# Kernel optimization log

Measured on AMD Instinct MI355X. Metric: run time of the kernel, lower is better.

The kernel has to match this reference:

```python
import jax, jax.numpy as jnp
import numpy as np

DN = ('NCHW', 'OIHW', 'NCHW')
EPS = 1e-5

def _conv(x, w, stride, padding):
    return jax.lax.conv_general_dilated(x, w, stride, padding, dimension_numbers=DN)

def _bn(x, g, b, m, v):
    # inference-mode BatchNorm2d
    s = g * jax.lax.rsqrt(v + EPS)
    return x * s[None, :, None, None] + (b - m * s)[None, :, None, None]

def _gn(x, g, b, groups):
    B, C, H, W = x.shape
    xr = x.reshape(B, groups, -1)
    mu = xr.mean(axis=2, keepdims=True)
    var = xr.var(axis=2, keepdims=True)
    xn = ((xr - mu) * jax.lax.rsqrt(var + EPS)).reshape(B, C, H, W)
    return xn * g[None, :, None, None] + b[None, :, None, None]

def _dsconv(f, ow, ob, og, obb, om, ov, w, wb, gg, gb, morph, k=3, extend_scope=1.0):
    B, C, H, W = f.shape
    S = H  # source DSC coordinate map only type-checks for square inputs
    off = jnp.tanh(_bn(_conv(f, ow, (1, 1), [(1, 1), (1, 1)]) + ob[None, :, None, None], og, obb, om, ov))
    # source passes y_offset for morph 0, x_offset for morph 1; both are added to y_new
    sel = off[:, :k] if morph == 0 else off[:, k:]
    center = k // 2
    # _apply_offset: detached clone, center zeroed; cumulative loop is empty for k=3
    off_cum = jax.lax.stop_gradient(sel).at[:, center].set(0.0) * extend_scope
    vals = jnp.linspace(float((-k) // 2), float(k // 2), k, dtype=f.dtype)  # [-2,-0.5,1] for k=3 (source quirk)
    rowc = jnp.arange(S, dtype=f.dtype)[:, None]  # both y_center and x_center equal the row index
    yg = jnp.zeros((k,), f.dtype) if morph == 0 else vals
    xg = vals if morph == 0 else jnp.zeros((k,), f.dtype)
    y = rowc[None, None] + yg[None, :, None, None] + off_cum                       # (B,k,S,S)
    x = jnp.broadcast_to(rowc[None, None] + xg[None, :, None, None], (B, k, S, S))
    rs = lambda t: t.transpose(0, 2, 1, 3).reshape(B, k * S, S)  # b p w h -> b (w p) h
    y, x = rs(y), rs(x)
    y0 = jnp.clip(jnp.floor(y), 0, S - 1); y1 = jnp.clip(jnp.floor(y) + 1.0, 0, S - 1)
    x0 = jnp.clip(jnp.floor(x), 0, S - 1); x1 = jnp.clip(jnp.floor(x) + 1.0, 0, S - 1)
    # source: index_a0 = base_y0 - base + x0  (batch offset cancels -> all batches gather from batch 0)
    flat0 = f[0].transpose(1, 2, 0).reshape(S * S, C)
    gat = lambda yy, xx: flat0[(yy * S + xx).astype(jnp.int32)]  # (B,kS,S,C)
    out = (gat(y0, x0) * ((y1 - y) * (x1 - x))[..., None]
         + gat(y0, x1) * ((y1 - y) * (x - x0))[..., None]
         + gat(y1, x0) * ((y - y0) * (x1 - x))[..., None]
         + gat(y1, x1) * ((y - y0) * (x - x0))[..., None])
    if morph == 0:
        df = out.transpose(0, 3, 1, 2)                    # (B,C,k*S,S)
        z = _conv(df, w, (k, 1), 'VALID')
    else:
        df = out.reshape(B, S, k * S, C).transpose(0, 3, 1, 2)  # (B,C,S,k*S)
        z = _conv(df, w, (1, k), 'VALID')
    z = z + wb[None, :, None, None]
    return jax.nn.silu(_gn(z, gg, gb, w.shape[0] // 4))

def _forward(x, w0, g0, b0, m0, v0,
             owx, obx, ogx, obbx, omx, ovx, wx, bwx, ggx, gbx,
             owy, oby, ogy, obby, omy, ovy, wy, bwy, ggy, gby):
    out0 = jax.nn.silu(_bn(_conv(x, w0, (1, 1), [(1, 1), (1, 1)]), g0, b0, m0, v0))
    outx = _dsconv(x, owx, obx, ogx, obbx, omx, ovx, wx, bwx, ggx, gbx, morph=0)
    outy = _dsconv(x, owy, oby, ogy, obby, omy, ovy, wy, bwy, ggy, gby, morph=1)
    return jnp.concatenate([out0, outx, outy], axis=1)

def setup_inputs() -> dict:
    B, C, O, S, K = 4, 64, 64, 256, 3
    key = jax.random.key(0)
    ks = jax.random.split(key, 32)
    rn = lambda i, sh, sc=1.0: jax.random.normal(ks[i], sh, dtype=jnp.float32) * sc
    ru = lambda i, sh: jax.random.uniform(ks[i], sh, dtype=jnp.float32) + 0.5
    return {
        'x': rn(0, (B, C, S, S)),
        'w0': rn(1, (O, C, 3, 3), 0.05), 'g0': ru(2, (O,)), 'b0': rn(3, (O,), 0.1),
        'm0': rn(4, (O,), 0.1), 'v0': ru(5, (O,)),
        'owx': rn(6, (2 * K, C, 3, 3), 0.05), 'obx': rn(7, (2 * K,), 0.1),
        'ogx': ru(8, (2 * K,)), 'obbx': rn(9, (2 * K,), 0.1), 'omx': rn(10, (2 * K,), 0.1), 'ovx': ru(11, (2 * K,)),
        'wx': rn(12, (O, C, K, 1), 0.05), 'bwx': rn(13, (O,), 0.1), 'ggx': ru(14, (O,)), 'gbx': rn(15, (O,), 0.1),
        'owy': rn(16, (2 * K, C, 3, 3), 0.05), 'oby': rn(17, (2 * K,), 0.1),
        'ogy': ru(18, (2 * K,)), 'obby': rn(19, (2 * K,), 0.1), 'omy': rn(20, (2 * K,), 0.1), 'ovy': ru(21, (2 * K,)),
        'wy': rn(22, (O, C, 1, K), 0.05), 'bwy': rn(23, (O,), 0.1), 'ggy': ru(24, (O,)), 'gby': rn(25, (O,), 0.1),
    }

def reference(x, w0, g0, b0, m0, v0,
              owx, obx, ogx, obbx, omx, ovx, wx, bwx, ggx, gbx,
              owy, oby, ogy, obby, omy, ovy, wy, bwy, ggy, gby):
    return _forward(x, w0, g0, b0, m0, v0,
                    owx, obx, ogx, obbx, omx, ovx, wx, bwx, ggx, gbx,
                    owy, oby, ogy, obby, omy, ovy, wy, bwy, ggy, gby)
```

## Files before the change

kernel.cpp:

```cpp
#include <hip/hip_runtime.h>
#include <hip/hip_bf16.h>
#include <math.h>

#define TS 256
#define HW 65536
#define CIN 64
#define EPSV 1e-5f
#define XPITCH 258

typedef __attribute__((ext_vector_type(8))) short bf16x8;
typedef __attribute__((ext_vector_type(4))) float f32x4;
typedef __attribute__((ext_vector_type(4))) unsigned short u16x4;
typedef unsigned short ushort_t;

__device__ __forceinline__ float silu_f(float v){ return v / (1.0f + expf(-v)); }
__device__ __forceinline__ ushort_t f2bf(float f){
    __hip_bfloat16 h = __float2bfloat16(f);
    return *reinterpret_cast<ushort_t*>(&h);
}
__device__ __forceinline__ float bf2f(ushort_t u){
    unsigned int t = ((unsigned int)u) << 16;
    return __uint_as_float(t);
}

__global__ __launch_bounds__(256) void k_xbf(const float* __restrict__ x, ushort_t* __restrict__ xbf){
    __shared__ float tile[64][65];
    int blk = blockIdx.x;
    int b = blk >> 10;
    int chunk = blk & 1023;
    int p0 = chunk * 64;
    int i = p0 >> 8, jb = p0 & 255;
    int tid = threadIdx.x;
    int lane = tid & 63, grp = tid >> 6;
    #pragma unroll
    for (int k = 0; k < 16; ++k){
        int c = k*4 + grp;
        tile[lane][c] = x[((size_t)(b*CIN + c))*HW + p0 + lane];
    }
    __syncthreads();
    #pragma unroll
    for (int k = 0; k < 16; ++k){
        int pp = k*4 + grp;
        xbf[(((size_t)b*258 + (i+1))*XPITCH + 1 + jb + pp)*64 + lane] = f2bf(tile[pp][lane]);
    }
}

__global__ void k_halo(ushort_t* __restrict__ xbf){
    int r = blockIdx.x;
    int b = blockIdx.y;
    int t = threadIdx.x;
    size_t rowbase = ((size_t)b*258 + r)*XPITCH*64;
    if (r == 0 || r == 257){
        for (int idx = t; idx < XPITCH*64; idx += 256) xbf[rowbase + idx] = 0;
    } else {
        if (t < 64) xbf[rowbase + t] = 0;
        else if (t < 128) xbf[rowbase + (size_t)257*64 + (t-64)] = 0;
    }
}

__global__ __launch_bounds__(256) void k_wrepack(const float* __restrict__ w0, ushort_t* __restrict__ w0bf){
    int idx = blockIdx.x*256 + threadIdx.x;
    int r = idx >> 12;
    int rem = idx & 4095;
    int o = rem >> 6, c = rem & 63;
    w0bf[idx] = f2bf(w0[(o*64 + c)*9 + r]);
}

__global__ __launch_bounds__(256) void k_wdsc(const float* __restrict__ wx, const float* __restrict__ wy,
        ushort_t* __restrict__ wbfx, ushort_t* __restrict__ wbfy){
    int idx = blockIdx.x*256 + threadIdx.x;
    int set = idx / 12288;
    int rem = idx - set*12288;
    int o = rem / 192;
    int k = rem - o*192;
    int t = k >> 6, c = k & 63;
    const float* w = set ? wy : wx;
    ushort_t* dst = set ? wbfy : wbfx;
    dst[rem] = f2bf(w[(o*64 + c)*3 + t]);
}

__global__ __launch_bounds__(256) void k_offp(const float* __restrict__ x,
        const float* __restrict__ owx, const float* __restrict__ owy,
        float* __restrict__ poff){
    __shared__ float xs[8][4][258];
    __shared__ float wsm[4][8][9];
    int by = blockIdx.y;
    int b = by >> 3, chunk = by & 7;
    int i0 = blockIdx.x * 2;
    int tid = threadIdx.x;
    for (int idx = tid; idx < 4*8*9; idx += 256){
        int o = idx / 72;
        int rem = idx - o*72;
        int c = rem / 9, tap = rem - c*9;
        int morph = o >> 1;
        int ch = (o==0)?0:(o==1)?2:(o==2)?3:5;
        const float* w = morph ? owy : owx;
        wsm[o][c][tap] = w[(ch*64 + chunk*8 + c)*9 + tap];
    }
    for (int idx = tid; idx < 8*4*258; idx += 256){
        int c = idx / 1032;
        int rem = idx - c*1032;
        int rr = rem / 258, col = rem - rr*258;
        int gy = i0 + rr - 1, gx = col - 1;
        float v = 0.f;
        if (gy >= 0 && gy < 256 && gx >= 0 && gx < 256)
            v = x[((size_t)(b*64 + chunk*8 + c))*HW + gy*256 + gx];
        xs[c][rr][col] = v;
    }
    __syncthreads();
    float acc[4][2];
    #pragma unroll
    for (int o = 0; o < 4; ++o){ acc[o][0]=0.f; acc[o][1]=0.f; }
    int j = tid;
    #pragma unroll
    for (int c = 0; c < 8; ++c){
        float vrow[4][3];
        #pragma unroll
        for (int rr = 0; rr < 4; ++rr){
            vrow[rr][0] = xs[c][rr][j];
            vrow[rr][1] = xs[c][rr][j+1];
            vrow[rr][2] = xs[c][rr][j+2];
        }
        #pragma unroll
        for (int o = 0; o < 4; ++o){
            const float* wr = wsm[o][c];
            #pragma unroll
            for (int ky = 0; ky < 3; ++ky){
                #pragma unroll
                for (int kx = 0; kx < 3; ++kx){
                    float wv = wr[ky*3+kx];
                    acc[o][0] += wv * vrow[ky][kx];
                    acc[o][1] += wv * vrow[ky+1][kx];
                }
            }
        }
    }
    #pragma unroll
    for (int o = 0; o < 4; ++o){
        size_t base = ((size_t)((chunk*4 + o)*4 + b))*HW;
        poff[base + (size_t)i0*256 + j]     = acc[o][0];
        poff[base + (size_t)(i0+1)*256 + j] = acc[o][1];
    }
}

__global__ __launch_bounds__(256) void k_offred(const float* __restrict__ poff,
        const float* __restrict__ ogx, const float* __restrict__ ovx,
        const float* __restrict__ obx, const float* __restrict__ omx,
        const float* __restrict__ obbx,
        const float* __restrict__ ogy, const float* __restrict__ ovy,
        const float* __restrict__ oby, const float* __restrict__ omy,
        const float* __restrict__ obby,
        float* __restrict__ off0, float* __restrict__ off1){
    int idx = blockIdx.x*256 + threadIdx.x;
    int px = idx & 65535;
    int t2 = idx >> 16;
    int b = t2 & 3;
    int o6 = t2 >> 2;
    if (o6 < 4){
        float s_ = 0.f;
        #pragma unroll
        for (int chunk = 0; chunk < 8; ++chunk)
            s_ += poff[((size_t)((chunk*4 + o6)*4 + b))*HW + px];
        int morph = o6 >> 1;
        int ch = (o6==0)?0:(o6==1)?2:(o6==2)?3:5;
        const float* og_ = morph? ogy:ogx; const float* ov_ = morph? ovy:ovx;
        const float* ob_ = morph? oby:obx; const float* om_ = morph? omy:omx;
        const float* obb_ = morph? obby:obbx;
        float sc = og_[ch]*rsqrtf(ov_[ch]+EPSV);
        float bi = (ob_[ch]-om_[ch])*sc + obb_[ch];
        int pl = (o6 & 1)*2;
        float* dst = (morph? off1:off0) + ((size_t)(b*3+pl))*HW;
        dst[px] = tanhf(s_*sc + bi);
    } else {
        float* dst = ((o6==5)? off1:off0) + ((size_t)(b*3+1))*HW;
        dst[px] = 0.f;
    }
}

__global__ __launch_bounds__(256) void k_conv0_mfma(
        const ushort_t* __restrict__ xbf, const ushort_t* __restrict__ w0bf,
        const float* __restrict__ g0, const float* __restrict__ b0,
        const float* __restrict__ m0, const float* __restrict__ v0,
        float* __restrict__ out){
    __shared__ __align__(16) ushort_t Xs[3*130*64];
    int jh = blockIdx.x;
    int i  = blockIdx.y;
    int b  = blockIdx.z;
    int tid = threadIdx.x;
    int j0h = jh*128;

    int wv = tid >> 6;
    int lane = tid & 63;
    int l15 = lane & 15;
    int lhi = lane >> 4;

    bf16x8 af[18];
    #pragma unroll
    for (int r = 0; r < 9; ++r)
        #pragma unroll
        for (int kc = 0; kc < 2; ++kc)
            af[r*2+kc] = *(const bf16x8*)(w0bf + (size_t)r*4096 + (wv*16 + l15)*64 + kc*32 + lhi*8);

    for (int idx = tid; idx < 3120; idx += 256){
        int rr = idx / 1040;
        int rem = idx - rr*1040;
        int p = rem >> 3, cgrp = rem & 7;
        bf16x8 v = *(const bf16x8*)(xbf + (((size_t)b*258 + (i + rr))*XPITCH + j0h + p)*64 + cgrp*8);
        int byte = rr*16640 + p*128 + ((cgrp*16) ^ ((p & 7) << 4));
        *(bf16x8*)((char*)Xs + byte) = v;
    }
    __syncthreads();

    f32x4 acc[8];
    #pragma unroll
    for (int ni = 0; ni < 8; ++ni) acc[ni] = (f32x4){0.f,0.f,0.f,0.f};

    #pragma unroll
    for (int ni = 0; ni < 8; ++ni){
        #pragma unroll
        for (int r = 0; r < 9; ++r){
            const int rr = r/3, dx = r%3 - 1;
            #pragma unroll
            for (int kc = 0; kc < 2; ++kc){
                int cb = kc*64 + lhi*16;
                int p = ni*16 + l15 + dx + 1;
                bf16x8 bfr = *(const bf16x8*)((char*)Xs + rr*16640 + p*128 + (cb ^ ((p & 7) << 4)));
                acc[ni] = __builtin_amdgcn_mfma_f32_16x16x32_bf16(af[r*2+kc], bfr, acc[ni], 0, 0, 0);
            }
        }
    }
    #pragma unroll
    for (int reg = 0; reg < 4; ++reg){
        int o = wv*16 + lhi*4 + reg;
        float s = g0[o] * rsqrtf(v0[o] + EPSV);
        float bi = b0[o] - m0[o]*s;
        #pragma unroll
        for (int ni = 0; ni < 8; ++ni){
            int j = jh*128 + ni*16 + l15;
            float v = acc[ni][reg]*s + bi;
            out[((size_t)(b*192 + o))*HW + i*TS + j] = silu_f(v);
        }
    }
}

template<int MORPH>
__global__ __launch_bounds__(256) void k_dsc2(const ushort_t* __restrict__ xbf, const float* __restrict__ offm,
        const ushort_t* __restrict__ wbf, const float* __restrict__ wb,
        float* __restrict__ outm, float* __restrict__ part){
    __shared__ __align__(16) ushort_t Vt[3*64*64];
    int b = blockIdx.z;
    int i = blockIdx.y;
    int j0 = blockIdx.x * 64;
    int tid = threadIdx.x;
    int lane16 = tid & 15;
    int pq = tid >> 4;
    const float fi = (float)i;

    #pragma unroll
    for (int it = 0; it < 12; ++it){
        int pair = it*16 + pq;
        int t = pair >> 6, jloc = pair & 63;
        float y, wx1, wx0;
        int x0i, x1i;
        if (MORPH == 0){
            int j = j0 + jloc;
            float off = offm[((size_t)(b*3 + t)*TS + i)*TS + j];
            y = fi + off;
            float vp = (t==0) ? -2.0f : ((t==1) ? -0.5f : 1.0f);
            float xf = fi + vp;
            float x0 = fminf(fmaxf(floorf(xf), 0.f), 255.f);
            float x1 = fminf(fmaxf(floorf(xf) + 1.f, 0.f), 255.f);
            wx1 = x1 - xf; wx0 = xf - x0;
            x0i = (int)x0; x1i = (int)x1;
        } else {
            int q = 3*(j0 + jloc) + t;
            int dl = q >> 8, jj = q & 255;
            float off = offm[((size_t)(b*3 + dl)*TS + i)*TS + jj];
            float vp = (dl==0) ? -2.0f : ((dl==1) ? -0.5f : 1.0f);
            y = fi + vp + off;
            wx1 = (i < 255) ? 1.f : 0.f; wx0 = 0.f;
            x0i = i; x1i = i;
        }
        float yf = floorf(y);
        float y0 = fminf(fmaxf(yf, 0.f), 255.f);
        float y1 = fminf(fmaxf(yf + 1.f, 0.f), 255.f);
        float wy1 = y1 - y, wy0 = y - y0;
        int y0i = (int)y0, y1i = (int)y1;
        int c0 = lane16*4;
        u16x4 a  = *(const u16x4*)(xbf + ((size_t)(y0i+1)*XPITCH + 1 + x0i)*64 + c0);
        u16x4 c_ = *(const u16x4*)(xbf + ((size_t)(y1i+1)*XPITCH + 1 + x0i)*64 + c0);
        float v[4];
        if (MORPH == 0 && wx0 != 0.f){
            u16x4 bv = *(const u16x4*)(xbf + ((size_t)(y0i+1)*XPITCH + 1 + x1i)*64 + c0);
            u16x4 d  = *(const u16x4*)(xbf + ((size_t)(y1i+1)*XPITCH + 1 + x1i)*64 + c0);
            #pragma unroll
            for (int k = 0; k < 4; ++k)
                v[k] = wy1*(wx1*bf2f(a[k]) + wx0*bf2f(bv[k]))
                     + wy0*(wx1*bf2f(c_[k]) + wx0*bf2f(d[k]));
        } else {
            #pragma unroll
            for (int k = 0; k < 4; ++k)
                v[k] = wx1*(wy1*bf2f(a[k]) + wy0*bf2f(c_[k]));
        }
        unsigned int lo = (unsigned int)f2bf(v[0]) | ((unsigned int)f2bf(v[1]) << 16);
        unsigned int hi = (unsigned int)f2bf(v[2]) | ((unsigned int)f2bf(v[3]) << 16);
        int cbyte = (c0*2) ^ ((jloc & 7) << 4);
        uint2 pk; pk.x = lo; pk.y = hi;
        *(uint2*)((char*)Vt + t*8192 + jloc*128 + cbyte) = pk;
    }
    __syncthreads();

    int wv = tid >> 6;
    int lane = tid & 63;
    int l15 = lane & 15, lhi = lane >> 4;
    int mi = wv;
    f32x4 acc[4];
    #pragma unroll
    for (int ni = 0; ni < 4; ++ni) acc[ni] = (f32x4){0.f,0.f,0.f,0.f};
    bf16x8 af[6];
    #pragma unroll
    for (int ks = 0; ks < 6; ++ks)
        af[ks] = *(const bf16x8*)(wbf + (mi*16 + l15)*192 + ks*32 + lhi*8);
    #pragma unroll
    for (int ks = 0; ks < 6; ++ks){
        int t = ks >> 1;
        int cbyte = ((ks & 1)*32 + lhi*8)*2;
        #pragma unroll
        for (int ni = 0; ni < 4; ++ni){
            int j = ni*16 + l15;
            bf16x8 bfr = *(const bf16x8*)((char*)Vt + t*8192 + j*128 + (cbyte ^ ((j & 7) << 4)));
            acc[ni] = __builtin_amdgcn_mfma_f32_16x16x32_bf16(af[ks], bfr, acc[ni], 0, 0, 0);
        }
    }
    float rsum[4], rsq[4];
    #pragma unroll
    for (int reg = 0; reg < 4; ++reg){
        int o = mi*16 + lhi*4 + reg;
        float bias = wb[o];
        float rs = 0.f, rq = 0.f;
        #pragma unroll
        for (int ni = 0; ni < 4; ++ni){
            int j = j0 + ni*16 + l15;
            float val = acc[ni][reg] + bias;
            outm[(size_t)b*192*HW + (size_t)o*HW + i*TS + j] = val;
            rs += val; rq += val*val;
        }
        #pragma unroll
        for (int m = 1; m < 16; m <<= 1){
            rs += __shfl_xor(rs, m, 64);
            rq += __shfl_xor(rq, m, 64);
        }
        rsum[reg] = rs; rsq[reg] = rq;
    }
    if (l15 == 0){
        float ts = rsum[0]+rsum[1]+rsum[2]+rsum[3];
        float tq = rsq[0]+rsq[1]+rsq[2]+rsq[3];
        int g = mi*4 + lhi;
        size_t slot = (((size_t)(MORPH*4 + b)*16 + g)*1024) + (blockIdx.y*4 + blockIdx.x);
        part[slot*2]   = ts;
        part[slot*2+1] = tq;
    }
}

__global__ __launch_bounds__(256) void k_gnfinal2(const float* __restrict__ part, float* __restrict__ stats){
    int slot = blockIdx.x;
    float s = 0.f, q = 0.f;
    for (int k = threadIdx.x; k < 1024; k += 256){
        s += part[((size_t)slot*1024 + k)*2];
        q += part[((size_t)slot*1024 + k)*2 + 1];
    }
    #pragma unroll
    for (int d = 32; d > 0; d >>= 1){ s += __shfl_down(s, d, 64); q += __shfl_down(q, d, 64); }
    __shared__ float rs[4], rq[4];
    int lane = threadIdx.x & 63, wv = threadIdx.x >> 6;
    if (lane == 0){ rs[wv] = s; rq[wv] = q; }
    __syncthreads();
    if (threadIdx.x == 0){
        float S = rs[0]+rs[1]+rs[2]+rs[3];
        float Q = rq[0]+rq[1]+rq[2]+rq[3];
        float inv = 1.f/262144.f;
        float mean = S*inv;
        float var = Q*inv - mean*mean;
        stats[slot*2] = mean;
        stats[slot*2+1] = rsqrtf(var + EPSV);
    }
}

__global__ __launch_bounds__(256) void k_gnapply(float* __restrict__ dout, const float* __restrict__ stats,
        const float* __restrict__ ggx, const float* __restrict__ gbx,
        const float* __restrict__ ggy, const float* __restrict__ gby){
    int idx = blockIdx.x*256 + threadIdx.x;
    int pix4 = idx & 16383;
    int chb = idx >> 14;
    int ch = chb & 127;
    int b = chb >> 7;
    int m = ch >> 6;
    int cc = ch & 63;
    int g = cc >> 2;
    const float* gg = m ? ggy : ggx;
    const float* gb = m ? gby : gbx;
    int si = ((m*4 + b)*16 + g)*2;
    float mean = stats[si], rsig = stats[si+1];
    float sc = rsig * gg[cc];
    float bi = gb[cc] - mean*sc;
    float4* ptr = (float4*)(dout + ((size_t)(b*192 + 64 + ch))*HW) + pix4;
    float4 v = *ptr;
    v.x = silu_f(v.x*sc + bi); v.y = silu_f(v.y*sc + bi);
    v.z = silu_f(v.z*sc + bi); v.w = silu_f(v.w*sc + bi);
    *ptr = v;
}

extern "C" void kernel_launch(void* const* d_in, const int* in_sizes, int n_in,
                              void* d_out, int out_size, void* d_ws, size_t ws_size,
                              hipStream_t stream){
    const float* x    = (const float*)d_in[0];
    const float* w0   = (const float*)d_in[1];
    const float* g0   = (const float*)d_in[2];
    const float* b0   = (const float*)d_in[3];
    const float* m0   = (const float*)d_in[4];
    const float* v0   = (const float*)d_in[5];
    const float* owx  = (const float*)d_in[6];
    const float* obx  = (const float*)d_in[7];
    const float* ogx  = (const float*)d_in[8];
    const float* obbx = (const float*)d_in[9];
    const float* omx  = (const float*)d_in[10];
    const float* ovx  = (const float*)d_in[11];
    const float* wx   = (const float*)d_in[12];
    const float* bwx  = (const float*)d_in[13];
    const float* ggx  = (const float*)d_in[14];
    const float* gbx  = (const float*)d_in[15];
    const float* owy  = (const float*)d_in[16];
    const float* oby  = (const float*)d_in[17];
    const float* ogy  = (const float*)d_in[18];
    const float* obby = (const float*)d_in[19];
    const float* omy  = (const float*)d_in[20];
    const float* ovy  = (const float*)d_in[21];
    const float* wy   = (const float*)d_in[22];
    const float* bwy  = (const float*)d_in[23];
    const float* ggy  = (const float*)d_in[24];
    const float* gby  = (const float*)d_in[25];

    float* out = (float*)d_out;
    ushort_t* xbf  = (ushort_t*)d_ws;
    ushort_t* w0bf = (ushort_t*)((char*)d_ws + 34078464);
    ushort_t* wbfx = (ushort_t*)((char*)d_ws + 34152192);
    ushort_t* wbfy = (ushort_t*)((char*)d_ws + 34176768);
    float* off0  = (float*)((char*)d_ws + 34201344);
    float* off1  = (float*)((char*)d_ws + 37347072);
    float* poff  = (float*)((char*)d_ws + 40492800);
    float* part  = (float*)((char*)d_ws + 40492800);
    float* stats = (float*)((char*)d_ws + 41541376);

    k_xbf<<<4096, 256, 0, stream>>>(x, xbf);
    k_halo<<<dim3(258,4), 256, 0, stream>>>(xbf);
    k_wrepack<<<144, 256, 0, stream>>>(w0, w0bf);
    k_wdsc<<<96, 256, 0, stream>>>(wx, wy, wbfx, wbfy);
    k_offp<<<dim3(128,32), 256, 0, stream>>>(x, owx, owy, poff);
    k_offred<<<6144, 256, 0, stream>>>(poff,
        ogx, ovx, obx, omx, obbx,
        ogy, ovy, oby, omy, obby,
        off0, off1);
    k_conv0_mfma<<<dim3(2,256,4), 256, 0, stream>>>(xbf, w0bf, g0, b0, m0, v0, out);
    k_dsc2<0><<<dim3(4,256,4), 256, 0, stream>>>(xbf, off0, wbfx, bwx, out + (size_t)64*HW, part);
    k_dsc2<1><<<dim3(4,256,4), 256, 0, stream>>>(xbf, off1, wbfy, bwy, out + (size_t)128*HW, part);
    k_gnfinal2<<<128, 256, 0, stream>>>(part, stats);
    k_gnapply<<<32768, 256, 0, stream>>>(out, stats, ggx, gbx, ggy, gby);
}
```

Baseline: 289.0 us.

## Retile conv0 MFMA waves, swizzle block order, stage DSC output in bf16

In conv0, each wave now computes a 2x4 tile of 16x16 outputs instead of 1x8. A single 16-pixel B fragment feeds two MFMAs, which halves LDS reads per MFMA, at the cost of holding twice the A-fragment registers. The grid is flattened with an XCD-aware swizzle of the block index, and launch bounds request two blocks per SIMD. The DSC branches now write pre-GroupNorm values to a bf16 scratch buffer rather than fp32 into the output, and run per-morph GN finalize/apply passes that read bf16 and write fp32. This lowers memory traffic on the intermediate but adds bf16 rounding before normalization and more launches.

Result: slower. 295.2 us (+2.1%).

```diff
diff --git a/kernel.cpp b/kernel.cpp
--- a/kernel.cpp
+++ b/kernel.cpp
@@ -177,15 +177,17 @@
     }
 }
 
-__global__ __launch_bounds__(256) void k_conv0_mfma(
+__global__ __launch_bounds__(256, 2) void k_conv0_mfma(
         const ushort_t* __restrict__ xbf, const ushort_t* __restrict__ w0bf,
         const float* __restrict__ g0, const float* __restrict__ b0,
         const float* __restrict__ m0, const float* __restrict__ v0,
         float* __restrict__ out){
     __shared__ __align__(16) ushort_t Xs[3*130*64];
-    int jh = blockIdx.x;
-    int i  = blockIdx.y;
-    int b  = blockIdx.z;
+    int id = blockIdx.x;
+    int id2 = ((id & 7) << 8) + (id >> 3);
+    int b  = id2 >> 9;
+    int i  = (id2 >> 1) & 255;
+    int jh = id2 & 1;
     int tid = threadIdx.x;
     int j0h = jh*128;
 
@@ -193,13 +195,17 @@
     int lane = tid & 63;
     int l15 = lane & 15;
     int lhi = lane >> 4;
-
-    bf16x8 af[18];
-    #pragma unroll
-    for (int r = 0; r < 9; ++r)
-        #pragma unroll
-        for (int kc = 0; kc < 2; ++kc)
-            af[r*2+kc] = *(const bf16x8*)(w0bf + (size_t)r*4096 + (wv*16 + l15)*64 + kc*32 + lhi*8);
+    int wmi = (wv >> 1) << 1;
+    int wni = (wv & 1) << 2;
+
+    bf16x8 af[2][18];
+    #pragma unroll
+    for (int m2 = 0; m2 < 2; ++m2)
+        #pragma unroll
+        for (int r = 0; r < 9; ++r)
+            #pragma unroll
+            for (int kc = 0; kc < 2; ++kc)
+                af[m2][r*2+kc] = *(const bf16x8*)(w0bf + (size_t)r*4096 + ((wmi+m2)*16 + l15)*64 + kc*32 + lhi*8);
 
     for (int idx = tid; idx < 3120; idx += 256){
         int rr = idx / 1040;
@@ -211,34 +217,41 @@
     }
     __syncthreads();
 
-    f32x4 acc[8];
-    #pragma unroll
-    for (int ni = 0; ni < 8; ++ni) acc[ni] = (f32x4){0.f,0.f,0.f,0.f};
-
-    #pragma unroll
-    for (int ni = 0; ni < 8; ++ni){
+    f32x4 acc[2][4];
+    #pragma unroll
+    for (int m2 = 0; m2 < 2; ++m2)
+        #pragma unroll
+        for (int ni = 0; ni < 4; ++ni)
+            acc[m2][ni] = (f32x4){0.f,0.f,0.f,0.f};
+
+    #pragma unroll
+    for (int ni = 0; ni < 4; ++ni){
         #pragma unroll
         for (int r = 0; r < 9; ++r){
             const int rr = r/3, dx = r%3 - 1;
             #pragma unroll
             for (int kc = 0; kc < 2; ++kc){
                 int cb = kc*64 + lhi*16;
-                int p = ni*16 + l15 + dx + 1;
+                int p = (wni+ni)*16 + l15 + dx + 1;
                 bf16x8 bfr = *(const bf16x8*)((char*)Xs + rr*16640 + p*128 + (cb ^ ((p & 7) << 4)));
-                acc[ni] = __builtin_amdgcn_mfma_f32_16x16x32_bf16(af[r*2+kc], bfr, acc[ni], 0, 0, 0);
+                acc[0][ni] = __builtin_amdgcn_mfma_f32_16x16x32_bf16(af[0][r*2+kc], bfr, acc[0][ni], 0, 0, 0);
+                acc[1][ni] = __builtin_amdgcn_mfma_f32_16x16x32_bf16(af[1][r*2+kc], bfr, acc[1][ni], 0, 0, 0);
             }
         }
     }
     #pragma unroll
-    for (int reg = 0; reg < 4; ++reg){
-        int o = wv*16 + lhi*4 + reg;
-        float s = g0[o] * rsqrtf(v0[o] + EPSV);
-        float bi = b0[o] - m0[o]*s;
-        #pragma unroll
-        for (int ni = 0; ni < 8; ++ni){
-            int j = jh*128 + ni*16 + l15;
-            float v = acc[ni][reg]*s + bi;
-            out[((size_t)(b*192 + o))*HW + i*TS + j] = silu_f(v);
+    for (int m2 = 0; m2 < 2; ++m2){
+        #pragma unroll
+        for (int reg = 0; reg < 4; ++reg){
+            int o = (wmi+m2)*16 + lhi*4 + reg;
+            float s = g0[o] * rsqrtf(v0[o] + EPSV);
+            float bi = b0[o] - m0[o]*s;
+            #pragma unroll
+            for (int ni = 0; ni < 4; ++ni){
+                int j = j0h + (wni+ni)*16 + l15;
+                float v = acc[m2][ni][reg]*s + bi;
+                out[((size_t)(b*192 + o))*HW + i*TS + j] = silu_f(v);
+            }
         }
     }
 }
@@ -246,7 +259,7 @@
 template<int MORPH>
 __global__ __launch_bounds__(256) void k_dsc2(const ushort_t* __restrict__ xbf, const float* __restrict__ offm,
         const ushort_t* __restrict__ wbf, const float* __restrict__ wb,
-        float* __restrict__ outm, float* __restrict__ part){
+        ushort_t* __restrict__ zb, float* __restrict__ part){
     __shared__ __align__(16) ushort_t Vt[3*64*64];
     int b = blockIdx.z;
     int i = blockIdx.y;
@@ -342,7 +355,7 @@
         for (int ni = 0; ni < 4; ++ni){
             int j = j0 + ni*16 + l15;
             float val = acc[ni][reg] + bias;
-            outm[(size_t)b*192*HW + (size_t)o*HW + i*TS + j] = val;
+            zb[((size_t)b*64 + o)*HW + i*TS + j] = f2bf(val);
             rs += val; rq += val*val;
         }
         #pragma unroll
@@ -356,7 +369,7 @@
         float ts = rsum[0]+rsum[1]+rsum[2]+rsum[3];
         float tq = rsq[0]+rsq[1]+rsq[2]+rsq[3];
         int g = mi*4 + lhi;
-        size_t slot = (((size_t)(MORPH*4 + b)*16 + g)*1024) + (blockIdx.y*4 + blockIdx.x);
+        size_t slot = (((size_t)b*16 + g)*1024) + (blockIdx.y*4 + blockIdx.x);
         part[slot*2]   = ts;
         part[slot*2+1] = tq;
     }
@@ -386,27 +399,26 @@
     }
 }
 
-__global__ __launch_bounds__(256) void k_gnapply(float* __restrict__ dout, const float* __restrict__ stats,
-        const float* __restrict__ ggx, const float* __restrict__ gbx,
-        const float* __restrict__ ggy, const float* __restrict__ gby){
+__global__ __launch_bounds__(256) void k_gnapply(float* __restrict__ dout, const ushort_t* __restrict__ zb,
+        const float* __restrict__ stats,
+        const float* __restrict__ gg, const float* __restrict__ gb, int m){
     int idx = blockIdx.x*256 + threadIdx.x;
     int pix4 = idx & 16383;
     int chb = idx >> 14;
-    int ch = chb & 127;
-    int b = chb >> 7;
-    int m = ch >> 6;
-    int cc = ch & 63;
+    int cc = chb & 63;
+    int b = chb >> 6;
     int g = cc >> 2;
-    const float* gg = m ? ggy : ggx;
-    const float* gb = m ? gby : gbx;
-    int si = ((m*4 + b)*16 + g)*2;
+    int si = (b*16 + g)*2;
     float mean = stats[si], rsig = stats[si+1];
     float sc = rsig * gg[cc];
     float bi = gb[cc] - mean*sc;
-    float4* ptr = (float4*)(dout + ((size_t)(b*192 + 64 + ch))*HW) + pix4;
-    float4 v = *ptr;
-    v.x = silu_f(v.x*sc + bi); v.y = silu_f(v.y*sc + bi);
-    v.z = silu_f(v.z*sc + bi); v.w = silu_f(v.w*sc + bi);
+    u16x4 zv = *(const u16x4*)(zb + ((size_t)(b*64 + cc))*HW + (size_t)pix4*4);
+    float4 v;
+    v.x = silu_f(bf2f(zv[0])*sc + bi);
+    v.y = silu_f(bf2f(zv[1])*sc + bi);
+    v.z = silu_f(bf2f(zv[2])*sc + bi);
+    v.w = silu_f(bf2f(zv[3])*sc + bi);
+    float4* ptr = (float4*)(dout + ((size_t)(b*192 + 64 + m*64 + cc))*HW) + pix4;
     *ptr = v;
 }
 
@@ -448,8 +460,9 @@
     float* off0  = (float*)((char*)d_ws + 34201344);
     float* off1  = (float*)((char*)d_ws + 37347072);
     float* poff  = (float*)((char*)d_ws + 40492800);
-    float* part  = (float*)((char*)d_ws + 40492800);
-    float* stats = (float*)((char*)d_ws + 41541376);
+    ushort_t* zbuf = (ushort_t*)((char*)d_ws + 40492800);
+    float* part  = (float*)((char*)d_ws + 74047232);
+    float* stats = (float*)((char*)d_ws + 74571520);
 
     k_xbf<<<4096, 256, 0, stream>>>(x, xbf);
     k_halo<<<dim3(258,4), 256, 0, stream>>>(xbf);
@@ -460,9 +473,11 @@
         ogx, ovx, obx, omx, obbx,
         ogy, ovy, oby, omy, obby,
         off0, off1);
-    k_conv0_mfma<<<dim3(2,256,4), 256, 0, stream>>>(xbf, w0bf, g0, b0, m0, v0, out);
-    k_dsc2<0><<<dim3(4,256,4), 256, 0, stream>>>(xbf, off0, wbfx, bwx, out + (size_t)64*HW, part);
-    k_dsc2<1><<<dim3(4,256,4), 256, 0, stream>>>(xbf, off1, wbfy, bwy, out + (size_t)128*HW, part);
-    k_gnfinal2<<<128, 256, 0, stream>>>(part, stats);
-    k_gnapply<<<32768, 256, 0, stream>>>(out, stats, ggx, gbx, ggy, gby);
-}
+    k_conv0_mfma<<<2048, 256, 0, stream>>>(xbf, w0bf, g0, b0, m0, v0, out);
+    k_dsc2<0><<<dim3(4,256,4), 256, 0, stream>>>(xbf, off0, wbfx, bwx, zbuf, part);
+    k_gnfinal2<<<64, 256, 0, stream>>>(part, stats);
+    k_gnapply<<<16384, 256, 0, stream>>>(out, zbuf, stats, ggx, gbx, 0);
+    k_dsc2<1><<<dim3(4,256,4), 256, 0, stream>>>(xbf, off1, wbfy, bwy, zbuf, part);
+    k_gnfinal2<<<64, 256, 0, stream>>>(part, stats + 128);
+    k_gnapply<<<16384, 256, 0, stream>>>(out, zbuf, stats + 128, ggy, gby, 1);
+}
```
